# Kernel optimization log

Hardware: AMD Instinct MI355X
Metric: run time of the kernel (lower is better)

The kernel has to match this reference:

```python
import jax, jax.numpy as jnp
import numpy as np

NCH, NBASIS, NXS, NF = 8, 30, 256, 200
NX = NXS * NXS * 2  # flattened real-pair k-space length


def _fft2c(z):
    # centered orthonormal 2D FFT over the last two axes
    z = jnp.fft.ifftshift(z, axes=(-2, -1))
    z = jnp.fft.fft2(z, norm='ortho')
    return jnp.fft.fftshift(z, axes=(-2, -1))


def setup_inputs() -> dict:
    key = jax.random.key(0)
    k1, k2, k3, k4 = jax.random.split(key, 4)
    x = jax.random.normal(k1, (NBASIS, NXS, NXS, 2), dtype=jnp.float32)
    csmT = jax.random.normal(k2, (NCH, NXS, NXS, 2), dtype=jnp.float32)
    VT = jax.random.normal(k3, (NBASIS, NF), dtype=jnp.float32)
    maskT = jax.random.randint(k4, (NF, NX), 0, 2).astype(jnp.bool_)
    return {"x": x, "csmT": csmT, "VT": VT, "maskT": maskT}


def reference(x, csmT, VT, maskT):
    # x: (nbasis, nx, nx, 2) real-pair complex; csmT: (nch, nx, nx, 2)
    xc = jax.lax.complex(x[..., 0], x[..., 1])          # (b, nx, nx)
    cc = jax.lax.complex(csmT[..., 0], csmT[..., 1])    # (c, nx, nx)
    # coil-sensitivity weighting + centered FFT, batched over all coils/basis
    Y = _fft2c(xc[None, :, :, :] * cc[:, None, :, :])   # (c, b, nx, nx) complex
    # interleave real/imag to match torch reshape of (..., nx, nx, 2) -> (..., NX)
    Yr = jnp.stack([Y.real, Y.imag], axis=-1).reshape(NCH, NBASIS, NX)
    # per-frame subspace projection then mask (mask commutes with the b-sum)
    out = maskT[None, :, :].astype(Yr.dtype) * jnp.einsum('cbn,bf->cfn', Yr, VT)
    return out  # (nch, NF, NX)
```

## Files before the change

### kernel.cpp

```cpp
#include <hip/hip_runtime.h>

#define NCH    8
#define NBASIS 30
#define NXS    256
#define NF     200
#define NX     (NXS*NXS*2)
#define NIMG   (NCH*NBASIS)
#define NFT    13
#define CPB    4

typedef float    f32x4  __attribute__((ext_vector_type(4)));
typedef unsigned u32x4  __attribute__((ext_vector_type(4)));
typedef short    bf16x8 __attribute__((ext_vector_type(8)));

__device__ __forceinline__ int bitrev8(int v) {
    return (int)(__builtin_bitreverse32((unsigned)v) >> 24);
}

__device__ __forceinline__ unsigned short f2bf(float f) {
    unsigned u = __float_as_uint(f);
    return (unsigned short)((u + 0x7FFFu + ((u >> 16) & 1u)) >> 16);
}

__global__ __launch_bounds__(256) void fft_rows_kernel(
        const float* __restrict__ x, const float* __restrict__ csm,
        unsigned short* __restrict__ Amid) {
    __shared__ float ldsRe[4][256];
    __shared__ float ldsIm[4][256];
    __shared__ float twRe[128], twIm[128];

    const int tid   = threadIdx.x;
    const int slice = tid >> 6;
    const int lane  = tid & 63;
    const int blk   = blockIdx.x;
    const int m     = blk >> 6;
    const int row   = ((blk & 63) << 2) + slice;
    const int c     = m / NBASIS;
    const int b     = m - c * NBASIS;

    if (tid < 128) {
        float a = (float)tid * (1.0f / 128.0f);
        twRe[tid] =  cospif(a);
        twIm[tid] = -sinpif(a);
    }

    const float* xr = x   + ((size_t)(b * NXS + row) * NXS) * 2;
    const float* cr = csm + ((size_t)(c * NXS + row) * NXS) * 2;
    #pragma unroll
    for (int j = 0; j < 4; ++j) {
        int col = lane + 64 * j;
        float2 xv = *(const float2*)(xr + col * 2);
        float2 cv = *(const float2*)(cr + col * 2);
        float s = ((row + col) & 1) ? -1.0f : 1.0f;
        ldsRe[slice][col] = s * (xv.x * cv.x - xv.y * cv.y);
        ldsIm[slice][col] = s * (xv.x * cv.y + xv.y * cv.x);
    }
    __syncthreads();

    #pragma unroll
    for (int half = 128; half >= 1; half >>= 1) {
        #pragma unroll
        for (int qq = 0; qq < 2; ++qq) {
            int q  = lane + 64 * qq;
            int g  = q / half;
            int j  = q - g * half;
            int i0 = g * 2 * half + j;
            int i1 = i0 + half;
            float ar = ldsRe[slice][i0], ai = ldsIm[slice][i0];
            float br = ldsRe[slice][i1], bi = ldsIm[slice][i1];
            ldsRe[slice][i0] = ar + br;
            ldsIm[slice][i0] = ai + bi;
            float dr = ar - br, di = ai - bi;
            int k = j * (128 / half);
            float wr = twRe[k], wi = twIm[k];
            ldsRe[slice][i1] = dr * wr - di * wi;
            ldsIm[slice][i1] = dr * wi + di * wr;
        }
        __syncthreads();
    }

    unsigned short* outp = Amid + (size_t)m * NX + (size_t)row * NXS * 2;
    #pragma unroll
    for (int j = 0; j < 4; ++j) {
        int k  = lane + 64 * j;
        int rk = bitrev8(k);
        unsigned pack = (unsigned)f2bf(ldsRe[slice][rk])
                      | ((unsigned)f2bf(ldsIm[slice][rk]) << 16);
        *(unsigned*)(outp + k * 2) = pack;
    }
}

#define CTILE 16
__global__ __launch_bounds__(256) void fft_cols_kernel(
        const unsigned short* __restrict__ Amid, unsigned short* __restrict__ Abf) {
    __shared__ float ldsRe[CTILE][257];
    __shared__ float ldsIm[CTILE][257];
    __shared__ float twRe[128], twIm[128];

    const int tid = threadIdx.x;
    const int blk = blockIdx.x;
    const int m   = blk >> 4;
    const int k0  = (blk & 15) * CTILE;

    if (tid < 128) {
        float a = (float)tid * (1.0f / 128.0f);
        twRe[tid] =  cospif(a);
        twIm[tid] = -sinpif(a);
    }

    const unsigned short* base = Amid + (size_t)m * NX;
    #pragma unroll
    for (int it = 0; it < 16; ++it) {
        int li = it * 256 + tid;
        int r  = li >> 4;
        int cc = li & 15;
        unsigned v = *(const unsigned*)(base + ((size_t)r * NXS + k0 + cc) * 2);
        ldsRe[cc][r] = __uint_as_float(v << 16);
        ldsIm[cc][r] = __uint_as_float(v & 0xFFFF0000u);
    }
    __syncthreads();

    const int slice = tid >> 6;
    const int lane  = tid & 63;

    #pragma unroll
    for (int half = 128; half >= 1; half >>= 1) {
        #pragma unroll
        for (int ci = 0; ci < 4; ++ci) {
            int col = slice * 4 + ci;
            #pragma unroll
            for (int qq = 0; qq < 2; ++qq) {
                int q  = lane + 64 * qq;
                int g  = q / half;
                int j  = q - g * half;
                int i0 = g * 2 * half + j;
                int i1 = i0 + half;
                float ar = ldsRe[col][i0], ai = ldsIm[col][i0];
                float br = ldsRe[col][i1], bi = ldsIm[col][i1];
                ldsRe[col][i0] = ar + br;
                ldsIm[col][i0] = ai + bi;
                float dr = ar - br, di = ai - bi;
                int k = j * (128 / half);
                float wr = twRe[k], wi = twIm[k];
                ldsRe[col][i1] = dr * wr - di * wi;
                ldsIm[col][i1] = dr * wi + di * wr;
            }
        }
        __syncthreads();
    }

    unsigned short* obase = Abf + (size_t)m * NX;
    #pragma unroll
    for (int it = 0; it < 16; ++it) {
        int li = it * 256 + tid;
        int ky = li >> 4;
        int cc = li & 15;
        int kx = k0 + cc;
        int rk = bitrev8(ky);
        float s = (((ky + kx) & 1) ? -1.0f : 1.0f) * (1.0f / 256.0f);
        unsigned pack = ((unsigned)f2bf(s * ldsIm[cc][rk]) << 16)
                      |  (unsigned)f2bf(s * ldsRe[cc][rk]);
        *(unsigned*)(obase + ((size_t)ky * NXS + kx) * 2) = pack;
    }
}

__global__ __launch_bounds__(256) void vt_prep_kernel(
        const float* __restrict__ VT, unsigned short* __restrict__ VTfrag) {
    int i = blockIdx.x * 256 + threadIdx.x;
    if (i >= NFT * 512) return;
    int ft = i >> 9, r = i & 511, lane = r >> 3, j = r & 7;
    int k = (lane >> 4) * 8 + j;
    int f = ft * 16 + (lane & 15);
    unsigned short v = 0;
    if (k < NBASIS && f < NF) v = f2bf(VT[k * NF + f]);
    VTfrag[i] = v;
}

__global__ __launch_bounds__(256) void project_mfma_kernel(
        const unsigned short* __restrict__ Abf,
        const unsigned short* __restrict__ VTfrag,
        const void*           __restrict__ maskT,
        float* __restrict__ out) {
    __shared__ __align__(16) unsigned char smem[4][4864];
    __shared__ __align__(16) unsigned short vtlds[NFT * 512];

    const int tid  = threadIdx.x;
    const int wv   = tid >> 6;
    const int lane = tid & 63;
    const int ksec = lane >> 4;
    const int fr   = lane & 15;
    const int c0   = blockIdx.y * CPB;
    const int n0w  = blockIdx.x * 256 + wv * 64;

    {
        const u32x4* src = (const u32x4*)VTfrag;
        u32x4*       dst = (u32x4*)vtlds;
        for (int i = tid; i < NFT * 512 / 8; i += 256) dst[i] = src[i];
    }

    const unsigned* mwd = (const unsigned*)maskT;
    bool byteMode = false;
    #pragma unroll
    for (int i = 0; i < 32; ++i) byteMode |= (mwd[i] > 1u);

    unsigned mbits[7] = {0u, 0u, 0u, 0u, 0u, 0u, 0u};
    if (byteMode) {
        const unsigned char* mb = (const unsigned char*)maskT + n0w + ksec * 4;
        #pragma unroll
        for (int ft = 0; ft < NFT; ++ft) {
            const int f_l = ft * 16 + fr;
            #pragma unroll
            for (int fn = 0; fn < 4; ++fn) {
                unsigned w = (f_l < NF)
                    ? *(const unsigned*)(mb + (size_t)f_l * NX + fn * 16) : 0u;
                unsigned nib = (w | (w >> 7) | (w >> 14) | (w >> 21)) & 0xFu;
                const int p = ft * 16 + fn * 4;
                mbits[p >> 5] |= nib << (p & 31);
            }
        }
    } else {
        const int* mi = (const int*)maskT + n0w + ksec * 4;
        #pragma unroll
        for (int ft = 0; ft < NFT; ++ft) {
            const int f_l = ft * 16 + fr;
            #pragma unroll
            for (int fn = 0; fn < 4; ++fn) {
                unsigned nib = 0u;
                if (f_l < NF) {
                    u32x4 v = *(const u32x4*)(mi + (size_t)f_l * NX + fn * 16);
                    nib = (v.x ? 1u : 0u) | (v.y ? 2u : 0u)
                        | (v.z ? 4u : 0u) | (v.w ? 8u : 0u);
                }
                const int p = ft * 16 + fn * 4;
                mbits[p >> 5] |= nib << (p & 31);
            }
        }
    }

    unsigned short (*ylds)[72] = (unsigned short (*)[72])smem[wv];
    float          (*ldsW)[68] = (float (*)[68])smem[wv];

    const int yrow = (lane >> 3) * 4;
    u32x4 ycur[4];
    {
        const unsigned short* src = Abf + (size_t)c0 * NBASIS * NX + n0w;
        #pragma unroll
        for (int i = 0; i < 4; ++i) {
            int idx = lane + 64 * i;
            int row = idx >> 3, seg = idx & 7;
            ycur[i] = (u32x4)(0u, 0u, 0u, 0u);
            if (row < NBASIS)
                ycur[i] = *(const u32x4*)(src + (size_t)row * NX + seg * 8);
        }
    }
    (void)yrow;

    __syncthreads();

    #pragma unroll 1
    for (int cc = 0; cc < CPB; ++cc) {
        const int c = c0 + cc;

        #pragma unroll
        for (int i = 0; i < 4; ++i) {
            int idx = lane + 64 * i;
            int row = idx >> 3, seg = idx & 7;
            *(u32x4*)&ylds[row][seg * 8] = ycur[i];
        }

        bf16x8 yfrag[4];
        #pragma unroll
        for (int fn = 0; fn < 4; ++fn) {
            #pragma unroll
            for (int j = 0; j < 8; ++j)
                yfrag[fn][j] = (short)ylds[ksec * 8 + j][fn * 16 + fr];
        }

        if (cc + 1 < CPB) {
            const unsigned short* src = Abf + (size_t)(c + 1) * NBASIS * NX + n0w;
            #pragma unroll
            for (int i = 0; i < 4; ++i) {
                int idx = lane + 64 * i;
                int row = idx >> 3, seg = idx & 7;
                u32x4 v = (u32x4)(0u, 0u, 0u, 0u);
                if (row < NBASIS)
                    v = *(const u32x4*)(src + (size_t)row * NX + seg * 8);
                ycur[i] = v;
            }
        }

        float* outc = out + (size_t)c * NF * NX;

        #pragma unroll
        for (int ft = 0; ft < NFT; ++ft) {
            bf16x8 vt = *(const bf16x8*)&vtlds[ft * 512 + lane * 8];

            #pragma unroll
            for (int fn = 0; fn < 4; ++fn) {
                const int p = ft * 16 + fn * 4;
                const unsigned nib = (mbits[p >> 5] >> (p & 31)) & 0xFu;
                f32x4 d = __builtin_amdgcn_mfma_f32_16x16x32_bf16(
                    yfrag[fn], vt, (f32x4)(0.f, 0.f, 0.f, 0.f), 0, 0, 0);
                f32x4 o;
                #pragma unroll
                for (int r = 0; r < 4; ++r)
                    o[r] = (nib & (1u << r)) ? d[r] : 0.0f;
                *(f32x4*)&ldsW[fr][fn * 16 + ksec * 4] = o;
            }

            #pragma unroll
            for (int rl = 0; rl < 4; ++rl) {
                int f_local = rl * 4 + ksec;
                int f = ft * 16 + f_local;
                f32x4 v = *(const f32x4*)&ldsW[f_local][fr * 4];
                if (f < NF)
                    __builtin_nontemporal_store(v,
                        (f32x4*)(outc + (size_t)f * NX + n0w + fr * 4));
            }
        }
    }
}

extern "C" void kernel_launch(void* const* d_in, const int* in_sizes, int n_in,
                              void* d_out, int out_size, void* d_ws, size_t ws_size,
                              hipStream_t stream) {
    const float* x    = (const float*)d_in[0];
    const float* csm  = (const float*)d_in[1];
    const float* VT   = (const float*)d_in[2];
    const void*  mask = d_in[3];
    float* out = (float*)d_out;

    char* ws = (char*)d_ws;
    unsigned short* Amid   = (unsigned short*)ws;
    unsigned short* Abf    = (unsigned short*)(ws + ((size_t)64 << 20));
    unsigned short* VTfrag = (unsigned short*)(ws + ((size_t)128 << 20));

    vt_prep_kernel<<<(NFT * 512 + 255) / 256, 256, 0, stream>>>(VT, VTfrag);
    fft_rows_kernel<<<NIMG * 64, 256, 0, stream>>>(x, csm, Amid);
    fft_cols_kernel<<<NIMG * 16, 256, 0, stream>>>(Amid, Abf);
    project_mfma_kernel<<<dim3(NX / 256, NCH / CPB), 256, 0, stream>>>(
        Abf, VTfrag, mask, out);
}
```

Baseline: 326.2 us.

## Share block-wide LDS staging so each wave stores full 1KB contiguous output rows

Replaces the per-wave LDS transpose buffer with one block-wide buffer covering 256 columns. Each wave then writes whole 1KB contiguous row segments of the output instead of 256-byte pieces, aiming for wider, more coalesced nontemporal stores on this store-bound kernel. In exchange it adds workgroup barriers around every frame-tile staging step and stops unrolling the frame-tile loop, which can serialize waves and reduce overlap.

Measured after the change: 331.4 us. No clear change (+1.6%).

```diff
diff --git a/kernel.cpp b/kernel.cpp
--- a/kernel.cpp
+++ b/kernel.cpp
@@ -181,7 +181,7 @@
         const unsigned short* __restrict__ VTfrag,
         const void*           __restrict__ maskT,
         float* __restrict__ out) {
-    __shared__ __align__(16) unsigned char smem[4][4864];
+    __shared__ __align__(16) unsigned char smem[19456];
     __shared__ __align__(16) unsigned short vtlds[NFT * 512];
 
     const int tid  = threadIdx.x;
@@ -190,7 +190,11 @@
     const int ksec = lane >> 4;
     const int fr   = lane & 15;
     const int c0   = blockIdx.y * CPB;
-    const int n0w  = blockIdx.x * 256 + wv * 64;
+    const int n0b  = blockIdx.x * 256;
+    const int n0w  = n0b + wv * 64;
+
+    unsigned short (*ylds)[72]  = (unsigned short (*)[72])(smem + wv * 4864);
+    float          (*ldsW)[268] = (float (*)[268])smem;
 
     {
         const u32x4* src = (const u32x4*)VTfrag;
@@ -237,10 +241,6 @@
         }
     }
 
-    unsigned short (*ylds)[72] = (unsigned short (*)[72])smem[wv];
-    float          (*ldsW)[68] = (float (*)[68])smem[wv];
-
-    const int yrow = (lane >> 3) * 4;
     u32x4 ycur[4];
     {
         const unsigned short* src = Abf + (size_t)c0 * NBASIS * NX + n0w;
@@ -253,7 +253,6 @@
                 ycur[i] = *(const u32x4*)(src + (size_t)row * NX + seg * 8);
         }
     }
-    (void)yrow;
 
     __syncthreads();
 
@@ -275,6 +274,10 @@
             for (int j = 0; j < 8; ++j)
                 yfrag[fn][j] = (short)ylds[ksec * 8 + j][fn * 16 + fr];
         }
+        asm volatile("s_waitcnt lgkmcnt(0)" ::: "memory");
+        __builtin_amdgcn_sched_barrier(0);
+        __builtin_amdgcn_s_barrier();
+        __builtin_amdgcn_sched_barrier(0);
 
         if (cc + 1 < CPB) {
             const unsigned short* src = Abf + (size_t)(c + 1) * NBASIS * NX + n0w;
@@ -291,7 +294,7 @@
 
         float* outc = out + (size_t)c * NF * NX;
 
-        #pragma unroll
+        #pragma unroll 1
         for (int ft = 0; ft < NFT; ++ft) {
             bf16x8 vt = *(const bf16x8*)&vtlds[ft * 512 + lane * 8];
 
@@ -305,18 +308,26 @@
                 #pragma unroll
                 for (int r = 0; r < 4; ++r)
                     o[r] = (nib & (1u << r)) ? d[r] : 0.0f;
-                *(f32x4*)&ldsW[fr][fn * 16 + ksec * 4] = o;
-            }
-
-            #pragma unroll
-            for (int rl = 0; rl < 4; ++rl) {
-                int f_local = rl * 4 + ksec;
+                *(f32x4*)&ldsW[fr][wv * 64 + fn * 16 + ksec * 4] = o;
+            }
+            asm volatile("s_waitcnt lgkmcnt(0)" ::: "memory");
+            __builtin_amdgcn_sched_barrier(0);
+            __builtin_amdgcn_s_barrier();
+            __builtin_amdgcn_sched_barrier(0);
+
+            #pragma unroll
+            for (int q = 0; q < 4; ++q) {
+                int f_local = wv * 4 + q;
                 int f = ft * 16 + f_local;
-                f32x4 v = *(const f32x4*)&ldsW[f_local][fr * 4];
+                f32x4 v = *(const f32x4*)&ldsW[f_local][lane * 4];
                 if (f < NF)
                     __builtin_nontemporal_store(v,
-                        (f32x4*)(outc + (size_t)f * NX + n0w + fr * 4));
-            }
+                        (f32x4*)(outc + (size_t)f * NX + n0b + lane * 4));
+            }
+            asm volatile("s_waitcnt lgkmcnt(0)" ::: "memory");
+            __builtin_amdgcn_sched_barrier(0);
+            __builtin_amdgcn_s_barrier();
+            __builtin_amdgcn_sched_barrier(0);
         }
     }
 }
```
